# Performance work log

Hardware: AMD Instinct MI355X
Metric: run time of the kernel (lower is better)

Reference implementation:

```python
import jax, jax.numpy as jnp
import numpy as np

N_HEADS = 16

def setup_inputs() -> dict:
    key = jax.random.key(0)
    qkv = jax.random.normal(key, (4, 3072, 1024), dtype=jnp.float32)
    return {"qkv": qkv}

def reference(qkv):
    bs, width, length = qkv.shape
    ch = width // (3 * N_HEADS)
    qkv_h = qkv.reshape(bs * N_HEADS, 3 * ch, length)
    q, k, v = jnp.split(qkv_h, 3, axis=1)  # each [bs*H, ch, T]
    scale = 1.0 / jnp.sqrt(jnp.sqrt(jnp.asarray(ch, qkv.dtype)))
    # [bs*H, T, T] scores
    weight = jnp.einsum('bct,bcs->bts', q * scale, k * scale)
    weight = jax.nn.softmax(weight.astype(jnp.float32), axis=-1).astype(weight.dtype)
    a = jnp.einsum('bts,bcs->bct', weight, v)  # [bs*H, ch, T]
    return a.reshape(bs, -1, length)
```

## Files before the change

### kernel.cpp

```cpp
#include <hip/hip_runtime.h>
#include <hip/hip_bf16.h>


typedef __bf16 bf16_8 __attribute__((ext_vector_type(8)));
typedef __bf16 bf16_4 __attribute__((ext_vector_type(4)));
typedef float floatx4 __attribute__((ext_vector_type(4)));

#define TSEQ 1024
#define BM 64
#define BN 64
#define NSTEPS 16
#define NTHREADS 256
#define STRIDE 72
#define OSTRIDE 68

#define LDS_BYTES 36864

__global__ __launch_bounds__(NTHREADS, 4)
void attn_kernel(const float* __restrict__ qkv, float* __restrict__ out) {
    __shared__ char smem[LDS_BYTES];
    __bf16* q_s = (__bf16*)smem;
    __bf16* k_s = (__bf16*)(smem + 9216);
    __bf16* v_s = (__bf16*)(smem + 18432);
    __bf16* p_s = (__bf16*)(smem + 27648);
    float*  o_s = (float*)smem;

    const int tid  = threadIdx.x;
    const int wave = tid >> 6;
    const int lane = tid & 63;
    const int quad = lane >> 4;
    const int i16  = lane & 15;

    const int bx = blockIdx.x;
    const int bh = bx & 63;
    const int t0 = (bx >> 6) * BM;

    const float* qg = qkv + (size_t)bh * 196608;
    const float* kg = qg + 65536;
    const float* vg = qg + 131072;

    int sc[4], ss4[4], sswz[4];
    #pragma unroll
    for (int j = 0; j < 4; ++j) {
        int f   = j * NTHREADS + tid;
        sc[j]   = f >> 4;
        ss4[j]  = (f & 15) << 2;
        sswz[j] = sc[j] ^ ((f & 7) << 3);
    }

    #pragma unroll
    for (int j = 0; j < 4; ++j) {
        float4 qv = *(const float4*)(qg + sc[j] * 1024 + t0 + ss4[j]);
        q_s[(ss4[j] + 0) * STRIDE + sswz[j]] = (__bf16)(qv.x * 0.125f);
        q_s[(ss4[j] + 1) * STRIDE + sswz[j]] = (__bf16)(qv.y * 0.125f);
        q_s[(ss4[j] + 2) * STRIDE + sswz[j]] = (__bf16)(qv.z * 0.125f);
        q_s[(ss4[j] + 3) * STRIDE + sswz[j]] = (__bf16)(qv.w * 0.125f);
        float4 kv = *(const float4*)(kg + sc[j] * 1024 + ss4[j]);
        k_s[(ss4[j] + 0) * STRIDE + sswz[j]] = (__bf16)kv.x;
        k_s[(ss4[j] + 1) * STRIDE + sswz[j]] = (__bf16)kv.y;
        k_s[(ss4[j] + 2) * STRIDE + sswz[j]] = (__bf16)kv.z;
        k_s[(ss4[j] + 3) * STRIDE + sswz[j]] = (__bf16)kv.w;
        float4 vv = *(const float4*)(vg + sc[j] * 1024 + ss4[j]);
        bf16_4 pv;
        pv[0] = (__bf16)vv.x; pv[1] = (__bf16)vv.y;
        pv[2] = (__bf16)vv.z; pv[3] = (__bf16)vv.w;
        *(bf16_4*)&v_s[sc[j] * STRIDE + ss4[j]] = pv;
    }
    __syncthreads();

    bf16_8 qf[2];
    {
        int row = wave * 16 + i16;
        int x = (row >> 2) & 7;
        #pragma unroll
        for (int kk = 0; kk < 2; ++kk)
            qf[kk] = *(const bf16_8*)&q_s[row * STRIDE + ((((kk << 2) | quad) ^ x) << 3)];
    }

    floatx4 O[4];
    #pragma unroll
    for (int cn = 0; cn < 4; ++cn) O[cn] = (floatx4){0.f, 0.f, 0.f, 0.f};
    float l[4] = {0.f, 0.f, 0.f, 0.f};

    for (int is = 0; is < NSTEPS; ++is) {
        float4 kr[4], vr[4];
        if (is < NSTEPS - 1) {
            const int s0n = (is + 1) * BN;
            #pragma unroll
            for (int j = 0; j < 4; ++j) {
                kr[j] = *(const float4*)(kg + sc[j] * 1024 + s0n + ss4[j]);
                vr[j] = *(const float4*)(vg + sc[j] * 1024 + s0n + ss4[j]);
            }
        }

        floatx4 S[4];
        #pragma unroll
        for (int n = 0; n < 4; ++n) {
            floatx4 acc = (floatx4){0.f, 0.f, 0.f, 0.f};
            int row = n * 16 + i16;
            int x = (row >> 2) & 7;
            #pragma unroll
            for (int kk = 0; kk < 2; ++kk) {
                bf16_8 kf = *(const bf16_8*)&k_s[row * STRIDE + ((((kk << 2) | quad) ^ x) << 3)];
                acc = __builtin_amdgcn_mfma_f32_16x16x32_bf16(qf[kk], kf, acc, 0, 0, 0);
            }
            S[n] = acc;
        }
        #pragma unroll
        for (int n = 0; n < 4; ++n)
            #pragma unroll
            for (int r = 0; r < 4; ++r) {
                float p = __expf(S[n][r]);
                S[n][r] = p;
                l[r] += p;
            }
        #pragma unroll
        for (int n = 0; n < 4; ++n)
            #pragma unroll
            for (int r = 0; r < 4; ++r)
                p_s[(wave * 16 + quad * 4 + r) * STRIDE + n * 16 + i16] = (__bf16)S[n][r];
        bf16_8 af[2];
        #pragma unroll
        for (int kk = 0; kk < 2; ++kk)
            af[kk] = *(const bf16_8*)&p_s[(wave * 16 + i16) * STRIDE + kk * 32 + quad * 8];
        #pragma unroll
        for (int cn = 0; cn < 4; ++cn)
            #pragma unroll
            for (int kk = 0; kk < 2; ++kk) {
                bf16_8 vf = *(const bf16_8*)&v_s[(cn * 16 + i16) * STRIDE + kk * 32 + quad * 8];
                O[cn] = __builtin_amdgcn_mfma_f32_16x16x32_bf16(af[kk], vf, O[cn], 0, 0, 0);
            }

        __syncthreads();
        if (is < NSTEPS - 1) {
            #pragma unroll
            for (int j = 0; j < 4; ++j) {
                k_s[(ss4[j] + 0) * STRIDE + sswz[j]] = (__bf16)kr[j].x;
                k_s[(ss4[j] + 1) * STRIDE + sswz[j]] = (__bf16)kr[j].y;
                k_s[(ss4[j] + 2) * STRIDE + sswz[j]] = (__bf16)kr[j].z;
                k_s[(ss4[j] + 3) * STRIDE + sswz[j]] = (__bf16)kr[j].w;
                bf16_4 pv;
                pv[0] = (__bf16)vr[j].x; pv[1] = (__bf16)vr[j].y;
                pv[2] = (__bf16)vr[j].z; pv[3] = (__bf16)vr[j].w;
                *(bf16_4*)&v_s[sc[j] * STRIDE + ss4[j]] = pv;
            }
        }
        __syncthreads();
    }

    float inv[4];
    #pragma unroll
    for (int r = 0; r < 4; ++r) {
        float s = l[r];
        #pragma unroll
        for (int off = 1; off < 16; off <<= 1)
            s += __shfl_xor(s, off);
        inv[r] = 1.0f / s;
    }

    __syncthreads();
    #pragma unroll
    for (int cn = 0; cn < 4; ++cn)
        #pragma unroll
        for (int r = 0; r < 4; ++r)
            o_s[(cn * 16 + i16) * OSTRIDE + wave * 16 + quad * 4 + r] = O[cn][r] * inv[r];
    __syncthreads();
    float* og = out + (size_t)bh * 65536 + t0;
    #pragma unroll
    for (int j = 0; j < 4; ++j)
        *(float4*)(og + sc[j] * 1024 + ss4[j]) = *(const float4*)&o_s[sc[j] * OSTRIDE + ss4[j]];
}

extern "C" void kernel_launch(void* const* d_in, const int* in_sizes, int n_in,
                              void* d_out, int out_size, void* d_ws, size_t ws_size,
                              hipStream_t stream) {
    const float* qkv = (const float*)d_in[0];
    float* out = (float*)d_out;
    attn_kernel<<<dim3(1024), dim3(NTHREADS), 0, stream>>>(qkv, out);
}
```

Before: 117.3 us.

## Double-buffer K/V tiles, use exp2 with folded scale, and store output directly

Double-buffers the K and V LDS tiles so each iteration needs one barrier instead of two, and reuses the Q region for the per-wave P scratch. Folds log2(e) into the Q scale so softmax uses the hardware exp2, and changes the LDS swizzles for K and P to cut bank conflicts. Swaps the MFMA operands so the output lands in a layout that can be written straight to global memory, dropping the LDS staging of O. LDS grows and occupancy drops to 3 blocks per CU, and the direct stores are 16-wide rather than float4.

```diff
diff --git a/kernel.cpp b/kernel.cpp
--- a/kernel.cpp
+++ b/kernel.cpp
@@ -6,24 +6,24 @@
 typedef __bf16 bf16_4 __attribute__((ext_vector_type(4)));
 typedef float floatx4 __attribute__((ext_vector_type(4)));
 
-#define TSEQ 1024
-#define BM 64
-#define BN 64
-#define NSTEPS 16
 #define NTHREADS 256
 #define STRIDE 72
-#define OSTRIDE 68
+#define NSTEPS 16
 
-#define LDS_BYTES 36864
+#if __has_builtin(__builtin_amdgcn_exp2f)
+#define EXP2(x) __builtin_amdgcn_exp2f(x)
+#else
+#define EXP2(x) exp2f(x)
+#endif
 
-__global__ __launch_bounds__(NTHREADS, 4)
+#define QSCALE 0.18033688011112042f
+
+#define LDS_BYTES 46080
+
+__global__ __launch_bounds__(NTHREADS, 3)
 void attn_kernel(const float* __restrict__ qkv, float* __restrict__ out) {
     __shared__ char smem[LDS_BYTES];
-    __bf16* q_s = (__bf16*)smem;
-    __bf16* k_s = (__bf16*)(smem + 9216);
-    __bf16* v_s = (__bf16*)(smem + 18432);
-    __bf16* p_s = (__bf16*)(smem + 27648);
-    float*  o_s = (float*)smem;
+    __bf16* qp_s = (__bf16*)smem;
 
     const int tid  = threadIdx.x;
     const int wave = tid >> 6;
@@ -33,48 +33,54 @@
 
     const int bx = blockIdx.x;
     const int bh = bx & 63;
-    const int t0 = (bx >> 6) * BM;
+    const int t0 = (bx >> 6) * 64;
 
     const float* qg = qkv + (size_t)bh * 196608;
     const float* kg = qg + 65536;
     const float* vg = qg + 131072;
 
-    int sc[4], ss4[4], sswz[4];
+    int sc[4], ss4[4], goff[4], kcol[4];
     #pragma unroll
     for (int j = 0; j < 4; ++j) {
         int f   = j * NTHREADS + tid;
         sc[j]   = f >> 4;
         ss4[j]  = (f & 15) << 2;
-        sswz[j] = sc[j] ^ ((f & 7) << 3);
+        goff[j] = sc[j] * 1024 + ss4[j];
+        kcol[j] = (((sc[j] >> 3) ^ ((ss4[j] >> 3) & 7)) << 3) | (sc[j] & 7);
     }
+
+    __bf16* k0 = (__bf16*)(smem + 9216);
+    __bf16* k1 = (__bf16*)(smem + 18432);
+    __bf16* v0 = (__bf16*)(smem + 27648);
+    __bf16* v1 = (__bf16*)(smem + 36864);
 
     #pragma unroll
     for (int j = 0; j < 4; ++j) {
-        float4 qv = *(const float4*)(qg + sc[j] * 1024 + t0 + ss4[j]);
-        q_s[(ss4[j] + 0) * STRIDE + sswz[j]] = (__bf16)(qv.x * 0.125f);
-        q_s[(ss4[j] + 1) * STRIDE + sswz[j]] = (__bf16)(qv.y * 0.125f);
-        q_s[(ss4[j] + 2) * STRIDE + sswz[j]] = (__bf16)(qv.z * 0.125f);
-        q_s[(ss4[j] + 3) * STRIDE + sswz[j]] = (__bf16)(qv.w * 0.125f);
-        float4 kv = *(const float4*)(kg + sc[j] * 1024 + ss4[j]);
-        k_s[(ss4[j] + 0) * STRIDE + sswz[j]] = (__bf16)kv.x;
-        k_s[(ss4[j] + 1) * STRIDE + sswz[j]] = (__bf16)kv.y;
-        k_s[(ss4[j] + 2) * STRIDE + sswz[j]] = (__bf16)kv.z;
-        k_s[(ss4[j] + 3) * STRIDE + sswz[j]] = (__bf16)kv.w;
-        float4 vv = *(const float4*)(vg + sc[j] * 1024 + ss4[j]);
+        float4 q4 = *(const float4*)(qg + goff[j] + t0);
+        qp_s[(ss4[j] + 0) * STRIDE + kcol[j]] = (__bf16)(q4.x * QSCALE);
+        qp_s[(ss4[j] + 1) * STRIDE + kcol[j]] = (__bf16)(q4.y * QSCALE);
+        qp_s[(ss4[j] + 2) * STRIDE + kcol[j]] = (__bf16)(q4.z * QSCALE);
+        qp_s[(ss4[j] + 3) * STRIDE + kcol[j]] = (__bf16)(q4.w * QSCALE);
+        float4 k4 = *(const float4*)(kg + goff[j]);
+        k0[(ss4[j] + 0) * STRIDE + kcol[j]] = (__bf16)k4.x;
+        k0[(ss4[j] + 1) * STRIDE + kcol[j]] = (__bf16)k4.y;
+        k0[(ss4[j] + 2) * STRIDE + kcol[j]] = (__bf16)k4.z;
+        k0[(ss4[j] + 3) * STRIDE + kcol[j]] = (__bf16)k4.w;
+        float4 v4 = *(const float4*)(vg + goff[j]);
         bf16_4 pv;
-        pv[0] = (__bf16)vv.x; pv[1] = (__bf16)vv.y;
-        pv[2] = (__bf16)vv.z; pv[3] = (__bf16)vv.w;
-        *(bf16_4*)&v_s[sc[j] * STRIDE + ss4[j]] = pv;
+        pv[0] = (__bf16)v4.x; pv[1] = (__bf16)v4.y;
+        pv[2] = (__bf16)v4.z; pv[3] = (__bf16)v4.w;
+        *(bf16_4*)&v0[sc[j] * STRIDE + ss4[j]] = pv;
     }
     __syncthreads();
 
     bf16_8 qf[2];
     {
         int row = wave * 16 + i16;
-        int x = (row >> 2) & 7;
+        int x = (row >> 3) & 7;
         #pragma unroll
         for (int kk = 0; kk < 2; ++kk)
-            qf[kk] = *(const bf16_8*)&q_s[row * STRIDE + ((((kk << 2) | quad) ^ x) << 3)];
+            qf[kk] = *(const bf16_8*)&qp_s[row * STRIDE + (((4 * kk + quad) ^ x) << 3)];
     }
 
     floatx4 O[4];
@@ -82,26 +88,32 @@
     for (int cn = 0; cn < 4; ++cn) O[cn] = (floatx4){0.f, 0.f, 0.f, 0.f};
     float l[4] = {0.f, 0.f, 0.f, 0.f};
 
+    const int pxw = (quad >> 1) << 1;
+    const int pxr = (i16 >> 3) << 1;
+    __bf16* pw = qp_s + (size_t)(wave * 16) * STRIDE;
+
     for (int is = 0; is < NSTEPS; ++is) {
         float4 kr[4], vr[4];
         if (is < NSTEPS - 1) {
-            const int s0n = (is + 1) * BN;
+            const int s0n = (is + 1) * 64;
             #pragma unroll
             for (int j = 0; j < 4; ++j) {
-                kr[j] = *(const float4*)(kg + sc[j] * 1024 + s0n + ss4[j]);
-                vr[j] = *(const float4*)(vg + sc[j] * 1024 + s0n + ss4[j]);
+                kr[j] = *(const float4*)(kg + goff[j] + s0n);
+                vr[j] = *(const float4*)(vg + goff[j] + s0n);
             }
         }
+        const __bf16* kc = (is & 1) ? k1 : k0;
+        const __bf16* vc = (is & 1) ? v1 : v0;
 
         floatx4 S[4];
         #pragma unroll
         for (int n = 0; n < 4; ++n) {
             floatx4 acc = (floatx4){0.f, 0.f, 0.f, 0.f};
             int row = n * 16 + i16;
-            int x = (row >> 2) & 7;
+            int x = (row >> 3) & 7;
             #pragma unroll
             for (int kk = 0; kk < 2; ++kk) {
-                bf16_8 kf = *(const bf16_8*)&k_s[row * STRIDE + ((((kk << 2) | quad) ^ x) << 3)];
+                bf16_8 kf = *(const bf16_8*)&kc[row * STRIDE + (((4 * kk + quad) ^ x) << 3)];
                 acc = __builtin_amdgcn_mfma_f32_16x16x32_bf16(qf[kk], kf, acc, 0, 0, 0);
             }
             S[n] = acc;
@@ -110,65 +122,72 @@
         for (int n = 0; n < 4; ++n)
             #pragma unroll
             for (int r = 0; r < 4; ++r) {
-                float p = __expf(S[n][r]);
+                float p = EXP2(S[n][r]);
                 S[n][r] = p;
                 l[r] += p;
             }
         #pragma unroll
-        for (int n = 0; n < 4; ++n)
+        for (int n = 0; n < 4; ++n) {
+            int g = ((2 * n + (i16 >> 3)) ^ pxw) << 3;
             #pragma unroll
             for (int r = 0; r < 4; ++r)
-                p_s[(wave * 16 + quad * 4 + r) * STRIDE + n * 16 + i16] = (__bf16)S[n][r];
+                pw[(4 * quad + r) * STRIDE + g + (i16 & 7)] = (__bf16)S[n][r];
+        }
         bf16_8 af[2];
         #pragma unroll
         for (int kk = 0; kk < 2; ++kk)
-            af[kk] = *(const bf16_8*)&p_s[(wave * 16 + i16) * STRIDE + kk * 32 + quad * 8];
+            af[kk] = *(const bf16_8*)&pw[i16 * STRIDE + (((4 * kk + quad) ^ pxr) << 3)];
         #pragma unroll
         for (int cn = 0; cn < 4; ++cn)
             #pragma unroll
             for (int kk = 0; kk < 2; ++kk) {
-                bf16_8 vf = *(const bf16_8*)&v_s[(cn * 16 + i16) * STRIDE + kk * 32 + quad * 8];
-                O[cn] = __builtin_amdgcn_mfma_f32_16x16x32_bf16(af[kk], vf, O[cn], 0, 0, 0);
+                bf16_8 vf = *(const bf16_8*)&vc[(cn * 16 + i16) * STRIDE + kk * 32 + quad * 8];
+                O[cn] = __builtin_amdgcn_mfma_f32_16x16x32_bf16(vf, af[kk], O[cn], 0, 0, 0);
             }
 
-        __syncthreads();
         if (is < NSTEPS - 1) {
+            __bf16* kn = (is & 1) ? k0 : k1;
+            __bf16* vn = (is & 1) ? v0 : v1;
             #pragma unroll
             for (int j = 0; j < 4; ++j) {
-                k_s[(ss4[j] + 0) * STRIDE + sswz[j]] = (__bf16)kr[j].x;
-                k_s[(ss4[j] + 1) * STRIDE + sswz[j]] = (__bf16)kr[j].y;
-                k_s[(ss4[j] + 2) * STRIDE + sswz[j]] = (__bf16)kr[j].z;
-                k_s[(ss4[j] + 3) * STRIDE + sswz[j]] = (__bf16)kr[j].w;
+                kn[(ss4[j] + 0) * STRIDE + kcol[j]] = (__bf16)kr[j].x;
+                kn[(ss4[j] + 1) * STRIDE + kcol[j]] = (__bf16)kr[j].y;
+                kn[(ss4[j] + 2) * STRIDE + kcol[j]] = (__bf16)kr[j].z;
+                kn[(ss4[j] + 3) * STRIDE + kcol[j]] = (__bf16)kr[j].w;
                 bf16_4 pv;
                 pv[0] = (__bf16)vr[j].x; pv[1] = (__bf16)vr[j].y;
                 pv[2] = (__bf16)vr[j].z; pv[3] = (__bf16)vr[j].w;
-                *(bf16_4*)&v_s[sc[j] * STRIDE + ss4[j]] = pv;
+                *(bf16_4*)&vn[sc[j] * STRIDE + ss4[j]] = pv;
             }
+            __syncthreads();
         }
-        __syncthreads();
     }
 
-    float inv[4];
-    #pragma unroll
-    for (int r = 0; r < 4; ++r) {
-        float s = l[r];
+    float linv;
+    {
+        float inv[4];
         #pragma unroll
-        for (int off = 1; off < 16; off <<= 1)
-            s += __shfl_xor(s, off);
-        inv[r] = 1.0f / s;
+        for (int r = 0; r < 4; ++r) {
+            float s = l[r];
+            #pragma unroll
+            for (int off = 1; off < 16; off <<= 1)
+                s += __shfl_xor(s, off);
+            inv[r] = 1.0f / s;
+        }
+        float* lf = (float*)(smem + wave * 16 * 144);
+        if (i16 == 0) {
+            #pragma unroll
+            for (int r = 0; r < 4; ++r) lf[4 * quad + r] = inv[r];
+        }
+        linv = lf[i16];
     }
 
-    __syncthreads();
+    float* og = out + (size_t)bh * 65536 + t0 + wave * 16;
     #pragma unroll
     for (int cn = 0; cn < 4; ++cn)
         #pragma unroll
         for (int r = 0; r < 4; ++r)
-            o_s[(cn * 16 + i16) * OSTRIDE + wave * 16 + quad * 4 + r] = O[cn][r] * inv[r];
-    __syncthreads();
-    float* og = out + (size_t)bh * 65536 + t0;
-    #pragma unroll
-    for (int j = 0; j < 4; ++j)
-        *(float4*)(og + sc[j] * 1024 + ss4[j]) = *(const float4*)&o_s[sc[j] * OSTRIDE + ss4[j]];
+            og[(cn * 16 + 4 * quad + r) * 1024 + i16] = O[cn][r] * linv;
 }
 
 extern "C" void kernel_launch(void* const* d_in, const int* in_sizes, int n_in,
```

Result: slower. 120.9 us (+3.0%).

## Double query tile per block, use transposed MFMA and exp2 softmax

Applied to the files above, without the earlier changes.

Each block now handles 128 query rows instead of 64, with every wave owning two 16-row tiles. This lets each K/V tile loaded into LDS serve twice as many queries and halves the grid size. Scores are computed in transposed form (K as the A operand), so probabilities can be written to LDS as packed 4-wide vectors. The softmax uses exp2 with the log2(e) factor folded into the Q scale. The output goes straight from registers to global memory without the LDS staging pass, and the trailing barrier in the last iteration is skipped. The costs are more registers per thread (launch bounds drop to 2 blocks per CU), only 512 blocks to spread across the GPU, and output stores that are less coalesced.

```diff
diff --git a/kernel.cpp b/kernel.cpp
--- a/kernel.cpp
+++ b/kernel.cpp
@@ -6,24 +6,25 @@
 typedef __bf16 bf16_4 __attribute__((ext_vector_type(4)));
 typedef float floatx4 __attribute__((ext_vector_type(4)));
 
-#define TSEQ 1024
-#define BM 64
-#define BN 64
-#define NSTEPS 16
 #define NTHREADS 256
 #define STRIDE 72
-#define OSTRIDE 68
+#define NSTEPS 16
+
+#if __has_builtin(__builtin_amdgcn_exp2f)
+#define EXP2(x) __builtin_amdgcn_exp2f(x)
+#else
+#define EXP2(x) exp2f(x)
+#endif
+#define QSCALE 0.18033688011112042f
 
 #define LDS_BYTES 36864
 
-__global__ __launch_bounds__(NTHREADS, 4)
+__global__ __launch_bounds__(NTHREADS, 2)
 void attn_kernel(const float* __restrict__ qkv, float* __restrict__ out) {
     __shared__ char smem[LDS_BYTES];
     __bf16* q_s = (__bf16*)smem;
-    __bf16* k_s = (__bf16*)(smem + 9216);
-    __bf16* v_s = (__bf16*)(smem + 18432);
-    __bf16* p_s = (__bf16*)(smem + 27648);
-    float*  o_s = (float*)smem;
+    __bf16* k_s = (__bf16*)(smem + 18432);
+    __bf16* v_s = (__bf16*)(smem + 27648);
 
     const int tid  = threadIdx.x;
     const int wave = tid >> 6;
@@ -33,142 +34,154 @@
 
     const int bx = blockIdx.x;
     const int bh = bx & 63;
-    const int t0 = (bx >> 6) * BM;
+    const int t0 = (bx >> 6) << 7;
 
     const float* qg = qkv + (size_t)bh * 196608;
     const float* kg = qg + 65536;
     const float* vg = qg + 131072;
 
-    int sc[4], ss4[4], sswz[4];
+    int sc[4], ss4[4], goff[4], swz[4];
     #pragma unroll
     for (int j = 0; j < 4; ++j) {
         int f   = j * NTHREADS + tid;
         sc[j]   = f >> 4;
         ss4[j]  = (f & 15) << 2;
-        sswz[j] = sc[j] ^ ((f & 7) << 3);
+        goff[j] = sc[j] * 1024 + ss4[j];
+        swz[j]  = sc[j] ^ ((f & 7) << 3);
     }
 
     #pragma unroll
+    for (int j = 0; j < 8; ++j) {
+        int f  = j * NTHREADS + tid;
+        int c  = f >> 5;
+        int t4 = (f & 31) << 2;
+        int sq = c ^ ((f & 7) << 3);
+        float4 q4 = *(const float4*)(qg + c * 1024 + t0 + t4);
+        q_s[(t4 + 0) * STRIDE + sq] = (__bf16)(q4.x * QSCALE);
+        q_s[(t4 + 1) * STRIDE + sq] = (__bf16)(q4.y * QSCALE);
+        q_s[(t4 + 2) * STRIDE + sq] = (__bf16)(q4.z * QSCALE);
+        q_s[(t4 + 3) * STRIDE + sq] = (__bf16)(q4.w * QSCALE);
+    }
+    #pragma unroll
     for (int j = 0; j < 4; ++j) {
-        float4 qv = *(const float4*)(qg + sc[j] * 1024 + t0 + ss4[j]);
-        q_s[(ss4[j] + 0) * STRIDE + sswz[j]] = (__bf16)(qv.x * 0.125f);
-        q_s[(ss4[j] + 1) * STRIDE + sswz[j]] = (__bf16)(qv.y * 0.125f);
-        q_s[(ss4[j] + 2) * STRIDE + sswz[j]] = (__bf16)(qv.z * 0.125f);
-        q_s[(ss4[j] + 3) * STRIDE + sswz[j]] = (__bf16)(qv.w * 0.125f);
-        float4 kv = *(const float4*)(kg + sc[j] * 1024 + ss4[j]);
-        k_s[(ss4[j] + 0) * STRIDE + sswz[j]] = (__bf16)kv.x;
-        k_s[(ss4[j] + 1) * STRIDE + sswz[j]] = (__bf16)kv.y;
-        k_s[(ss4[j] + 2) * STRIDE + sswz[j]] = (__bf16)kv.z;
-        k_s[(ss4[j] + 3) * STRIDE + sswz[j]] = (__bf16)kv.w;
-        float4 vv = *(const float4*)(vg + sc[j] * 1024 + ss4[j]);
+        float4 k4 = *(const float4*)(kg + goff[j]);
+        k_s[(ss4[j] + 0) * STRIDE + swz[j]] = (__bf16)k4.x;
+        k_s[(ss4[j] + 1) * STRIDE + swz[j]] = (__bf16)k4.y;
+        k_s[(ss4[j] + 2) * STRIDE + swz[j]] = (__bf16)k4.z;
+        k_s[(ss4[j] + 3) * STRIDE + swz[j]] = (__bf16)k4.w;
+        float4 v4 = *(const float4*)(vg + goff[j]);
         bf16_4 pv;
-        pv[0] = (__bf16)vv.x; pv[1] = (__bf16)vv.y;
-        pv[2] = (__bf16)vv.z; pv[3] = (__bf16)vv.w;
+        pv[0] = (__bf16)v4.x; pv[1] = (__bf16)v4.y;
+        pv[2] = (__bf16)v4.z; pv[3] = (__bf16)v4.w;
         *(bf16_4*)&v_s[sc[j] * STRIDE + ss4[j]] = pv;
     }
     __syncthreads();
 
-    bf16_8 qf[2];
-    {
-        int row = wave * 16 + i16;
+    bf16_8 qf[2][2];
+    #pragma unroll
+    for (int tt = 0; tt < 2; ++tt) {
+        int row = wave * 32 + tt * 16 + i16;
         int x = (row >> 2) & 7;
         #pragma unroll
         for (int kk = 0; kk < 2; ++kk)
-            qf[kk] = *(const bf16_8*)&q_s[row * STRIDE + ((((kk << 2) | quad) ^ x) << 3)];
+            qf[tt][kk] = *(const bf16_8*)&q_s[row * STRIDE + ((((kk << 2) | quad) ^ x) << 3)];
     }
 
-    floatx4 O[4];
+    floatx4 O[2][4];
     #pragma unroll
-    for (int cn = 0; cn < 4; ++cn) O[cn] = (floatx4){0.f, 0.f, 0.f, 0.f};
-    float l[4] = {0.f, 0.f, 0.f, 0.f};
+    for (int tt = 0; tt < 2; ++tt)
+        #pragma unroll
+        for (int cn = 0; cn < 4; ++cn) O[tt][cn] = (floatx4){0.f, 0.f, 0.f, 0.f};
+    float l[2] = {0.f, 0.f};
+
+    __bf16* pw = q_s + (size_t)(wave * 32) * STRIDE;
 
     for (int is = 0; is < NSTEPS; ++is) {
         float4 kr[4], vr[4];
         if (is < NSTEPS - 1) {
-            const int s0n = (is + 1) * BN;
+            const int s0n = (is + 1) * 64;
             #pragma unroll
             for (int j = 0; j < 4; ++j) {
-                kr[j] = *(const float4*)(kg + sc[j] * 1024 + s0n + ss4[j]);
-                vr[j] = *(const float4*)(vg + sc[j] * 1024 + s0n + ss4[j]);
+                kr[j] = *(const float4*)(kg + goff[j] + s0n);
+                vr[j] = *(const float4*)(vg + goff[j] + s0n);
             }
         }
 
-        floatx4 S[4];
+        floatx4 St[2][4];
         #pragma unroll
-        for (int n = 0; n < 4; ++n) {
-            floatx4 acc = (floatx4){0.f, 0.f, 0.f, 0.f};
-            int row = n * 16 + i16;
+        for (int sb = 0; sb < 4; ++sb) {
+            floatx4 a0 = (floatx4){0.f, 0.f, 0.f, 0.f};
+            floatx4 a1 = (floatx4){0.f, 0.f, 0.f, 0.f};
+            int row = sb * 16 + i16;
             int x = (row >> 2) & 7;
             #pragma unroll
             for (int kk = 0; kk < 2; ++kk) {
                 bf16_8 kf = *(const bf16_8*)&k_s[row * STRIDE + ((((kk << 2) | quad) ^ x) << 3)];
-                acc = __builtin_amdgcn_mfma_f32_16x16x32_bf16(qf[kk], kf, acc, 0, 0, 0);
+                a0 = __builtin_amdgcn_mfma_f32_16x16x32_bf16(kf, qf[0][kk], a0, 0, 0, 0);
+                a1 = __builtin_amdgcn_mfma_f32_16x16x32_bf16(kf, qf[1][kk], a1, 0, 0, 0);
             }
-            S[n] = acc;
+            St[0][sb] = a0;
+            St[1][sb] = a1;
         }
         #pragma unroll
-        for (int n = 0; n < 4; ++n)
+        for (int tt = 0; tt < 2; ++tt)
             #pragma unroll
-            for (int r = 0; r < 4; ++r) {
-                float p = __expf(S[n][r]);
-                S[n][r] = p;
-                l[r] += p;
+            for (int sb = 0; sb < 4; ++sb) {
+                float p0 = EXP2(St[tt][sb][0]);
+                float p1 = EXP2(St[tt][sb][1]);
+                float p2 = EXP2(St[tt][sb][2]);
+                float p3 = EXP2(St[tt][sb][3]);
+                l[tt] += (p0 + p1) + (p2 + p3);
+                bf16_4 pk;
+                pk[0] = (__bf16)p0; pk[1] = (__bf16)p1;
+                pk[2] = (__bf16)p2; pk[3] = (__bf16)p3;
+                *(bf16_4*)&pw[(tt * 16 + i16) * STRIDE + sb * 16 + quad * 4] = pk;
             }
+        bf16_8 af[2][2];
         #pragma unroll
-        for (int n = 0; n < 4; ++n)
+        for (int tt = 0; tt < 2; ++tt)
             #pragma unroll
-            for (int r = 0; r < 4; ++r)
-                p_s[(wave * 16 + quad * 4 + r) * STRIDE + n * 16 + i16] = (__bf16)S[n][r];
-        bf16_8 af[2];
-        #pragma unroll
-        for (int kk = 0; kk < 2; ++kk)
-            af[kk] = *(const bf16_8*)&p_s[(wave * 16 + i16) * STRIDE + kk * 32 + quad * 8];
+            for (int kk = 0; kk < 2; ++kk)
+                af[tt][kk] = *(const bf16_8*)&pw[(tt * 16 + i16) * STRIDE + kk * 32 + quad * 8];
         #pragma unroll
         for (int cn = 0; cn < 4; ++cn)
             #pragma unroll
             for (int kk = 0; kk < 2; ++kk) {
                 bf16_8 vf = *(const bf16_8*)&v_s[(cn * 16 + i16) * STRIDE + kk * 32 + quad * 8];
-                O[cn] = __builtin_amdgcn_mfma_f32_16x16x32_bf16(af[kk], vf, O[cn], 0, 0, 0);
+                O[0][cn] = __builtin_amdgcn_mfma_f32_16x16x32_bf16(vf, af[0][kk], O[0][cn], 0, 0, 0);
+                O[1][cn] = __builtin_amdgcn_mfma_f32_16x16x32_bf16(vf, af[1][kk], O[1][cn], 0, 0, 0);
             }
 
-        __syncthreads();
         if (is < NSTEPS - 1) {
+            __syncthreads();
             #pragma unroll
             for (int j = 0; j < 4; ++j) {
-                k_s[(ss4[j] + 0) * STRIDE + sswz[j]] = (__bf16)kr[j].x;
-                k_s[(ss4[j] + 1) * STRIDE + sswz[j]] = (__bf16)kr[j].y;
-                k_s[(ss4[j] + 2) * STRIDE + sswz[j]] = (__bf16)kr[j].z;
-                k_s[(ss4[j] + 3) * STRIDE + sswz[j]] = (__bf16)kr[j].w;
+                k_s[(ss4[j] + 0) * STRIDE + swz[j]] = (__bf16)kr[j].x;
+                k_s[(ss4[j] + 1) * STRIDE + swz[j]] = (__bf16)kr[j].y;
+                k_s[(ss4[j] + 2) * STRIDE + swz[j]] = (__bf16)kr[j].z;
+                k_s[(ss4[j] + 3) * STRIDE + swz[j]] = (__bf16)kr[j].w;
                 bf16_4 pv;
                 pv[0] = (__bf16)vr[j].x; pv[1] = (__bf16)vr[j].y;
                 pv[2] = (__bf16)vr[j].z; pv[3] = (__bf16)vr[j].w;
                 *(bf16_4*)&v_s[sc[j] * STRIDE + ss4[j]] = pv;
             }
+            __syncthreads();
         }
-        __syncthreads();
     }
 
-    float inv[4];
+    float* og = out + (size_t)bh * 65536 + t0 + wave * 32;
     #pragma unroll
-    for (int r = 0; r < 4; ++r) {
-        float s = l[r];
+    for (int tt = 0; tt < 2; ++tt) {
+        float s = l[tt];
+        s += __shfl_xor(s, 16);
+        s += __shfl_xor(s, 32);
+        const float linv = 1.0f / s;
         #pragma unroll
-        for (int off = 1; off < 16; off <<= 1)
-            s += __shfl_xor(s, off);
-        inv[r] = 1.0f / s;
+        for (int cn = 0; cn < 4; ++cn)
+            #pragma unroll
+            for (int r = 0; r < 4; ++r)
+                og[(cn * 16 + 4 * quad + r) * 1024 + tt * 16 + i16] = O[tt][cn][r] * linv;
     }
-
-    __syncthreads();
-    #pragma unroll
-    for (int cn = 0; cn < 4; ++cn)
-        #pragma unroll
-        for (int r = 0; r < 4; ++r)
-            o_s[(cn * 16 + i16) * OSTRIDE + wave * 16 + quad * 4 + r] = O[cn][r] * inv[r];
-    __syncthreads();
-    float* og = out + (size_t)bh * 65536 + t0;
-    #pragma unroll
-    for (int j = 0; j < 4; ++j)
-        *(float4*)(og + sc[j] * 1024 + ss4[j]) = *(const float4*)&o_s[sc[j] * OSTRIDE + ss4[j]];
 }
 
 extern "C" void kernel_launch(void* const* d_in, const int* in_sizes, int n_in,
@@ -176,5 +189,5 @@
                               hipStream_t stream) {
     const float* qkv = (const float*)d_in[0];
     float* out = (float*)d_out;
-    attn_kernel<<<dim3(1024), dim3(NTHREADS), 0, stream>>>(qkv, out);
+    attn_kernel<<<dim3(512), dim3(NTHREADS), 0, stream>>>(qkv, out);
 }
```

Result: faster. 109.7 us (-6.5%).
